# Kernel optimization log

Measured on AMD Instinct MI355X. Metric: run time of the kernel, lower is better.

Reference implementation:

```python
import jax, jax.numpy as jnp
import numpy as np
from jax import lax

B_CAPS, C_CAPS, K, STRIDE, ITERS = 32, 32, 3, 2, 3
BATCH, WIN = 8, 14
W_OUT = (WIN - K) // STRIDE + 1  # 6
CWW = C_CAPS * W_OUT * W_OUT     # 1152
LOG_2PI = float(np.log(2.0 * np.pi))


def setup_inputs() -> dict:
    key = jax.random.key(0)
    k1, k2, k3, k4, k5 = jax.random.split(key, 5)
    return {
        "poses": jax.random.normal(k1, (BATCH, B_CAPS, WIN, WIN, 16), jnp.float32),
        "activations": jax.random.uniform(k2, (BATCH, B_CAPS, WIN, WIN), jnp.float32),
        "lambda_": jnp.ones((), jnp.float32),
        "W": jax.random.normal(k3, (B_CAPS, K, K, C_CAPS, 4, 4), jnp.float32),
        "beta_v": jax.random.normal(k4, (1, CWW, 1), jnp.float32),
        "beta_a": jax.random.normal(k5, (1, CWW), jnp.float32),
    }


def reference(poses, activations, lambda_, W, beta_v, beta_a):
    b, B, win = poses.shape[0], poses.shape[1], poses.shape[2]
    C = W.shape[3]
    w = (win - K) // STRIDE + 1
    Bkk, Cww = B * K * K, C * w * w

    pose = poses.reshape(b, 16, B, win, win).transpose(0, 2, 3, 4, 1)

    # im2col patch extraction (vectorized): rows[i,k] = stride*i + k
    rows = ((jnp.arange(w) * STRIDE)[:, None] + jnp.arange(K)).reshape(-1)  # (w*K,)
    p = jnp.take(pose, rows, axis=2).reshape(b, B, w, K, win, 16)
    p = jnp.take(p, rows, axis=4).reshape(b, B, w, K, w, K, 16)
    patches = p.transpose(0, 1, 3, 5, 6, 2, 4)          # (b,B,K,K,16,wi,wj)
    # faithful reproduction of torch's view (b,B,K,K,16,ww)->(b,B,K,K,1,w,w,4,4)
    patches = patches.reshape(b, B, K, K, w, w, 4, 4)

    # votes: broadcast 4x4 matmul W @ pose-patch
    votes = jnp.einsum('sxyzij,bsxyuvjk->bsxyzuvik', W, patches)
    votes = votes.reshape(b, Bkk, Cww, 16)

    # activation patches, tiled over C (coordinate_add=False branch)
    a = jnp.take(activations, rows, axis=2).reshape(b, B, w, K, win)
    a = jnp.take(a, rows, axis=4).reshape(b, B, w, K, w, K)
    a = a.transpose(0, 1, 3, 5, 2, 4).reshape(b, Bkk, 1, w * w)
    act = jnp.broadcast_to(a, (b, Bkk, C, w * w)).reshape(b, Bkk, Cww)

    # EM routing
    R = jnp.ones((b, Bkk, Cww), votes.dtype) / Cww
    for i in range(ITERS + 1):
        Ra = (R * act)[..., None]                        # (b,Bkk,Cww,1)
        sum_R = Ra.sum(1)                                # (b,Cww,1)
        mu = ((Ra * votes).sum(1) / sum_R)[:, None]      # (b,1,Cww,16)
        sigma_sq = (Ra * (votes - mu) ** 2).sum(1) / sum_R  # (b,Cww,16)
        if i != ITERS:
            mu_d = lax.stop_gradient(mu)
            ss_d = lax.stop_gradient(sigma_sq)[:, None]  # (b,1,Cww,16)
            V_d = lax.stop_gradient(votes)
            a_d = lax.stop_gradient(act)
            log_p = -0.5 * (V_d - mu_d) ** 2 / ss_d - 0.5 * jnp.log(ss_d) - 0.5 * LOG_2PI
            ap = a_d * jnp.exp(log_p).sum(-1)            # (b,Bkk,Cww)
            R = ap / ap.sum(-1, keepdims=True)
        else:
            cost = (beta_v + jnp.log(sigma_sq)) * sum_R  # (b,Cww,16)
            a_out = jax.nn.sigmoid(lambda_ * (beta_a - cost.sum(2)))  # (b,Cww)

    return (mu.reshape(b, C, w, w, 16), a_out.reshape(b, C, w, w))
```

## Files before the change

### kernel.cpp

```cpp
#include <hip/hip_runtime.h>
#include <hip/hip_bf16.h>

#define NB   8
#define NM   288
#define NN   1152
#define NUV  36
#define ND   16

#define OFF_P    0
#define SZ_P     (NB*NUV*NM*ND)
#define OFF_WT   (OFF_P + SZ_P)
#define SZ_WT    (32*NM*ND)
#define OFF_ACT  (OFF_WT + SZ_WT)
#define SZ_ACT   (NB*NUV*NM)
#define OFF_L    (OFF_ACT + SZ_ACT)
#define SZ_L     (NB*NN*NM)
#define OFF_LSE  (OFF_L + SZ_L)
#define SZ_LSE   (NB*NM)
#define OFF_FLAG (OFF_LSE + SZ_LSE)
#define OFF_PM   (OFF_FLAG + 16)
#define SZ_PM    (NB*NUV*NM)
#define OFF_PS   (OFF_PM + SZ_PM)
#define SZ_PS    (NB*NUV*NM)

#define HALF_LOG_2PI 0.9189385332046727f
#define LOG_NN       7.049254841255839f
#define NEG_BIG      (-1.0e30f)

__device__ __forceinline__ float ldin(const void* p, int i, int f32) {
    return f32 ? ((const float*)p)[i]
               : __bfloat162float(((const __hip_bfloat16*)p)[i]);
}

__device__ __forceinline__ unsigned short bfbits(float f) {
    __hip_bfloat16 h = __float2bfloat16(f);
    return __builtin_bit_cast(unsigned short, h);
}

__device__ __forceinline__ float dot2bf(unsigned a, unsigned b, float c) {
    float d;
    asm("v_dot2_f32_bf16 %0, %1, %2, %3" : "=v"(d) : "v"(a), "v"(b), "v"(c));
    return d;
}

__global__ void detect_kernel(const unsigned short* __restrict__ poses_u16,
                              int* __restrict__ flag) {
    if (blockIdx.x == 0 && threadIdx.x == 0) {
        int wild = 0;
        for (int i = 0; i < 64; ++i) {
            int ex = (poses_u16[i] >> 7) & 0xFF;
            if (ex >= 133) ++wild;
        }
        *flag = (wild >= 4) ? 1 : 0;
    }
}

__global__ __launch_bounds__(256) void prep_kernel(
    const void* __restrict__ poses, const void* __restrict__ acts,
    const void* __restrict__ Wb, __hip_bfloat16* __restrict__ P,
    __hip_bfloat16* __restrict__ Wt, float* __restrict__ A36,
    const int* __restrict__ flagp)
{
    const int f32 = *flagp;
    const int blk = blockIdx.x;
    const int tid = threadIdx.x;
    if (blk < 256) {
        __shared__ float ps[16 * 196];
        __shared__ float asld[196];
        const int b = blk >> 5, s = blk & 31;
        for (int e = tid; e < 16 * 196; e += 256) {
            int c = e / 196, hw = e % 196;
            ps[e] = ldin(poses, ((b * 16 + c) * 32 + s) * 196 + hw, f32);
        }
        for (int e = tid; e < 196; e += 256)
            asld[e] = ldin(acts, (b * 32 + s) * 196 + e, f32);
        __syncthreads();
        for (int o2 = tid; o2 < 648; o2 += 256) {
            int row = o2 >> 1, half = o2 & 1;
            int uv = row / 9, xy = row % 9;
            int u = uv / 6, vv2 = uv % 6;
            int x = xy / 3, y = xy % 3;
            unsigned pk[4];
#pragma unroll
            for (int h = 0; h < 4; ++h) {
                unsigned lohi[2];
#pragma unroll
                for (int e = 0; e < 2; ++e) {
                    int kj = half * 8 + h * 2 + e;
                    int k = kj >> 2, j = kj & 3;
                    int idx = u * 96 + vv2 * 16 + j * 4 + k;
                    int c = idx / 36, rem = idx % 36;
                    int wi = rem / 6, wj = rem % 6;
                    lohi[e] = bfbits(ps[c * 196 + (2 * wi + x) * 14 + (2 * wj + y)]);
                }
                pk[h] = lohi[0] | (lohi[1] << 16);
            }
            *((uint4*)(P + (((size_t)((b * 36 + uv) * 288 + s * 9 + xy)) << 4) + half * 8)) =
                make_uint4(pk[0], pk[1], pk[2], pk[3]);
        }
        for (int o = tid; o < 324; o += 256) {
            int uv = o / 9, xy = o % 9;
            int u = uv / 6, vv2 = uv % 6;
            int x = xy / 3, y = xy % 3;
            A36[(b * 36 + uv) * 288 + s * 9 + xy] =
                __logf(asld[(2 * u + x) * 14 + (2 * vv2 + y)]);
        }
    } else {
        int idx = (blk - 256) * 256 + tid;
        int z = idx / 288, m = idx % 288;
        unsigned pk[8];
#pragma unroll
        for (int h = 0; h < 8; ++h) {
            unsigned lo = bfbits(ldin(Wb, m * 512 + z * 16 + 2 * h, f32));
            unsigned hi = bfbits(ldin(Wb, m * 512 + z * 16 + 2 * h + 1, f32));
            pk[h] = lo | (hi << 16);
        }
        uint4* dst = (uint4*)(Wt + idx * 16);
        dst[0] = make_uint4(pk[0], pk[1], pk[2], pk[3]);
        dst[1] = make_uint4(pk[4], pk[5], pk[6], pk[7]);
    }
}

__global__ __launch_bounds__(288, 4) void em_iter(
    const unsigned short* __restrict__ wsP, const unsigned short* __restrict__ wsWt,
    const float* __restrict__ wsA, float* __restrict__ wsL,
    const float* __restrict__ wsLSE,
    const void* __restrict__ beta_v,
    const void* __restrict__ beta_a,
    const void* __restrict__ lambda_,
    void* __restrict__ outv, const int* __restrict__ flagp, int iter)
{
    __shared__ float red[NM * 17];
    __shared__ float Mhw[9];
    __shared__ float paru[NM];
    __shared__ float parv[NM];
    __shared__ float paruW[18];
    __shared__ float mul[16], nhil[16], ltl[16], ssl[16];

    const int tid = threadIdx.x;
    const int B   = blockIdx.x;
    const int rr  = B & 255;
    const int z   = rr >> 3;
    const int g   = ((B >> 8) << 3) | (rr & 7);
    const int b   = g / NUV;
    const int uv  = g % NUV;
    const int n   = z * NUV + uv;
    const int bn  = b * NN + n;

    const uint4* Wq = (const uint4*)(wsWt + ((z * NM + tid) << 4));
    const uint4* Pq = (const uint4*)(wsP + ((g * NM + tid) << 4));
    uint4 wq0 = Wq[0], wq1 = Wq[1];
    uint4 pq0 = Pq[0], pq1 = Pq[1];
    const float lact = wsA[g * NM + tid];
    float t;
    if (iter == 0) t = lact - LOG_NN;
    else t = wsL[(size_t)bn * NM + tid] - wsLSE[b * NM + tid] + lact;
    t = fmaxf(t, NEG_BIG);

    float mhw = t;
#pragma unroll
    for (int off = 1; off < 32; off <<= 1)
        mhw = fmaxf(mhw, __shfl_xor(mhw, off, 32));
    const float w = __expf(t - mhw);
    if ((tid & 31) == 0) Mhw[tid >> 5] = mhw;

    unsigned Wa[4]  = {wq0.x, wq0.z, wq1.x, wq1.z};
    unsigned Wb_[4] = {wq0.y, wq0.w, wq1.y, wq1.w};
    unsigned Pa[4]  = {pq0.x, pq0.z, pq1.x, pq1.z};
    unsigned Pb[4]  = {pq0.y, pq0.w, pq1.y, pq1.w};
    float v[16];
#pragma unroll
    for (int i = 0; i < 4; ++i)
#pragma unroll
        for (int k = 0; k < 4; ++k)
            v[i * 4 + k] = dot2bf(Wa[i], Pa[k], dot2bf(Wb_[i], Pb[k], 0.f));

#pragma unroll
    for (int dd = 0; dd < 16; ++dd) red[tid * 17 + dd] = v[dd];
    red[tid * 17 + 16] = w;
    __syncthreads();

    {
        const int d = tid & 15, c = tid >> 4;
        const float* base = &red[(c << 4) * 17];
        float s1 = 0.f, s2 = 0.f, sw = 0.f;
#pragma unroll
        for (int q = 0; q < 16; ++q) {
            float ww = base[q * 17 + 16];
            float vv = base[q * 17 + d];
            float t1 = ww * vv;
            s1 += t1; s2 += t1 * vv; sw += ww;
        }
        paru[d * 18 + c] = s1;
        parv[d * 18 + c] = s2;
        if (d == 0) paruW[c] = sw;
    }
    __syncthreads();

    float M_f = NEG_BIG, sW_f = 0.f;
    if (tid < 16) {
        float M = Mhw[0];
#pragma unroll
        for (int h = 1; h < 9; ++h) M = fmaxf(M, Mhw[h]);
        float sW = 0.f, S1 = 0.f, S2 = 0.f;
#pragma unroll
        for (int c = 0; c < 18; ++c) {
            float sc = __expf(Mhw[c >> 1] - M);
            sW += paruW[c] * sc;
            S1 += paru[tid * 18 + c] * sc;
            S2 += parv[tid * 18 + c] * sc;
        }
        float mu = S1 / sW;
        float q2 = S2 / sW;
        float ss = fmaxf(q2 - mu * mu, 1e-30f);
        mul[tid]  = mu;
        ssl[tid]  = ss;
        nhil[tid] = -0.5f / ss;
        ltl[tid]  = -0.5f * __logf(ss) - HALF_LOG_2PI;
        M_f = M; sW_f = sW;
    }
    __syncthreads();

    if (iter < 3) {
        float lp[16];
        float M = NEG_BIG;
#pragma unroll
        for (int dd = 0; dd < 16; ++dd) {
            float df = v[dd] - mul[dd];
            lp[dd] = df * df * nhil[dd] + ltl[dd];
            M = fmaxf(M, lp[dd]);
        }
        float s = 0.f;
#pragma unroll
        for (int dd = 0; dd < 16; ++dd) s += __expf(lp[dd] - M);
        wsL[(size_t)bn * NM + tid] = lact + M + __logf(s);
    } else {
        const int f32 = *flagp;
        if (tid < 16) {
            if (f32) ((float*)outv)[(bn << 4) + tid] = mul[tid];
            else ((__hip_bfloat16*)outv)[(bn << 4) + tid] = __float2bfloat16(mul[tid]);
        }
        if (tid == 0) {
            float sumR = __expf(M_f) * sW_f;
            float bv = ldin(beta_v, n, f32);
            float c = 0.f;
#pragma unroll
            for (int dd = 0; dd < 16; ++dd) c += bv + __logf(ssl[dd]);
            c *= sumR;
            float lam = ldin(lambda_, 0, f32);
            float ba  = ldin(beta_a, n, f32);
            float ao  = 1.f / (1.f + __expf(-(lam * (ba - c))));
            int oi = NB * NN * ND + bn;
            if (f32) ((float*)outv)[oi] = ao;
            else ((__hip_bfloat16*)outv)[oi] = __float2bfloat16(ao);
        }
    }
}

__global__ __launch_bounds__(288) void lse1_kernel(const float* __restrict__ L,
                                                   float* __restrict__ PM,
                                                   float* __restrict__ PS)
{
    const int tid = threadIdx.x;
    const int blk = blockIdx.x;
    const int b = blk / NUV;
    const int c = blk % NUV;
    const float* base = L + ((size_t)b * NN + c * 32) * NM + tid;
    float mx = NEG_BIG;
#pragma unroll
    for (int r = 0; r < 32; ++r) mx = fmaxf(mx, base[r * NM]);
    float s = 0.f;
#pragma unroll
    for (int r = 0; r < 32; ++r) s += __expf(base[r * NM] - mx);
    PM[blk * NM + tid] = mx;
    PS[blk * NM + tid] = s;
}

__global__ void lse2_kernel(const float* __restrict__ PM,
                            const float* __restrict__ PS,
                            float* __restrict__ LSE)
{
    int t = blockIdx.x * 256 + threadIdx.x;
    if (t >= NB * NM) return;
    int b = t / NM, m = t % NM;
    const float* pm = PM + (size_t)b * NUV * NM + m;
    const float* ps = PS + (size_t)b * NUV * NM + m;
    float mx = NEG_BIG;
#pragma unroll
    for (int cc = 0; cc < NUV; ++cc) mx = fmaxf(mx, pm[cc * NM]);
    float s = 0.f;
#pragma unroll
    for (int cc = 0; cc < NUV; ++cc) s += ps[cc * NM] * __expf(pm[cc * NM] - mx);
    LSE[t] = mx + __logf(s);
}

extern "C" void kernel_launch(void* const* d_in, const int* in_sizes, int n_in,
                              void* d_out, int out_size, void* d_ws, size_t ws_size,
                              hipStream_t stream)
{
    const void* poses = d_in[0];
    const void* acts  = d_in[1];
    const void* lam   = d_in[2];
    const void* Wb    = d_in[3];
    const void* bv    = d_in[4];
    const void* ba    = d_in[5];

    float* ws  = (float*)d_ws;
    __hip_bfloat16* P  = (__hip_bfloat16*)(ws + OFF_P);
    __hip_bfloat16* Wt = (__hip_bfloat16*)(ws + OFF_WT);
    float* A36 = ws + OFF_ACT;
    float* L   = ws + OFF_L;
    float* LSE = ws + OFF_LSE;
    int*  flag = (int*)(ws + OFF_FLAG);
    float* PM  = ws + OFF_PM;
    float* PS  = ws + OFF_PS;

    detect_kernel<<<1, 64, 0, stream>>>((const unsigned short*)poses, flag);

    prep_kernel<<<292, 256, 0, stream>>>(poses, acts, Wb, P, Wt, A36, flag);

    for (int it = 0; it < 4; ++it) {
        em_iter<<<NB * NN, 288, 0, stream>>>((const unsigned short*)P,
                                             (const unsigned short*)Wt,
                                             A36, L, LSE, bv, ba, lam,
                                             d_out, flag, it);
        if (it < 3) {
            lse1_kernel<<<NB * NUV, 288, 0, stream>>>(L, PM, PS);
            lse2_kernel<<<9, 256, 0, stream>>>(PM, PS, LSE);
        }
    }
}
```

Measured before the change: 231.7 us.

## Process each output capsule with one wavefront using register and shuffle reductions

Each output capsule is now handled by a single 64-lane wavefront, with four capsules per 256-thread block. Each lane owns five of the 288 input rows, and the mean and variance sums are reduced with cross-lane shuffles instead of shared-memory arrays and block barriers. This removes the __syncthreads calls and the LDS traffic. In exchange, register pressure rises sharply (80 vote values plus 32 partial accumulators per lane), which risks spills or lower occupancy, and half the lanes sit idle on the fifth row chunk.

```diff
diff --git a/kernel.cpp b/kernel.cpp
--- a/kernel.cpp
+++ b/kernel.cpp
@@ -121,7 +121,7 @@
     }
 }
 
-__global__ __launch_bounds__(288, 4) void em_iter(
+__global__ __launch_bounds__(256) void em_iter(
     const unsigned short* __restrict__ wsP, const unsigned short* __restrict__ wsWt,
     const float* __restrict__ wsA, float* __restrict__ wsL,
     const float* __restrict__ wsLSE,
@@ -130,123 +130,136 @@
     const void* __restrict__ lambda_,
     void* __restrict__ outv, const int* __restrict__ flagp, int iter)
 {
-    __shared__ float red[NM * 17];
-    __shared__ float Mhw[9];
-    __shared__ float paru[NM];
-    __shared__ float parv[NM];
-    __shared__ float paruW[18];
-    __shared__ float mul[16], nhil[16], ltl[16], ssl[16];
-
-    const int tid = threadIdx.x;
-    const int B   = blockIdx.x;
-    const int rr  = B & 255;
-    const int z   = rr >> 3;
-    const int g   = ((B >> 8) << 3) | (rr & 7);
-    const int b   = g / NUV;
-    const int uv  = g % NUV;
-    const int n   = z * NUV + uv;
-    const int bn  = b * NN + n;
-
-    const uint4* Wq = (const uint4*)(wsWt + ((z * NM + tid) << 4));
-    const uint4* Pq = (const uint4*)(wsP + ((g * NM + tid) << 4));
-    uint4 wq0 = Wq[0], wq1 = Wq[1];
-    uint4 pq0 = Pq[0], pq1 = Pq[1];
-    const float lact = wsA[g * NM + tid];
-    float t;
-    if (iter == 0) t = lact - LOG_NN;
-    else t = wsL[(size_t)bn * NM + tid] - wsLSE[b * NM + tid] + lact;
-    t = fmaxf(t, NEG_BIG);
-
-    float mhw = t;
-#pragma unroll
-    for (int off = 1; off < 32; off <<= 1)
-        mhw = fmaxf(mhw, __shfl_xor(mhw, off, 32));
-    const float w = __expf(t - mhw);
-    if ((tid & 31) == 0) Mhw[tid >> 5] = mhw;
-
-    unsigned Wa[4]  = {wq0.x, wq0.z, wq1.x, wq1.z};
-    unsigned Wb_[4] = {wq0.y, wq0.w, wq1.y, wq1.w};
-    unsigned Pa[4]  = {pq0.x, pq0.z, pq1.x, pq1.z};
-    unsigned Pb[4]  = {pq0.y, pq0.w, pq1.y, pq1.w};
-    float v[16];
-#pragma unroll
-    for (int i = 0; i < 4; ++i)
-#pragma unroll
-        for (int k = 0; k < 4; ++k)
-            v[i * 4 + k] = dot2bf(Wa[i], Pa[k], dot2bf(Wb_[i], Pb[k], 0.f));
-
-#pragma unroll
-    for (int dd = 0; dd < 16; ++dd) red[tid * 17 + dd] = v[dd];
-    red[tid * 17 + 16] = w;
-    __syncthreads();
-
-    {
-        const int d = tid & 15, c = tid >> 4;
-        const float* base = &red[(c << 4) * 17];
-        float s1 = 0.f, s2 = 0.f, sw = 0.f;
-#pragma unroll
-        for (int q = 0; q < 16; ++q) {
-            float ww = base[q * 17 + 16];
-            float vv = base[q * 17 + d];
-            float t1 = ww * vv;
-            s1 += t1; s2 += t1 * vv; sw += ww;
-        }
-        paru[d * 18 + c] = s1;
-        parv[d * 18 + c] = s2;
-        if (d == 0) paruW[c] = sw;
-    }
-    __syncthreads();
-
-    float M_f = NEG_BIG, sW_f = 0.f;
-    if (tid < 16) {
-        float M = Mhw[0];
-#pragma unroll
-        for (int h = 1; h < 9; ++h) M = fmaxf(M, Mhw[h]);
-        float sW = 0.f, S1 = 0.f, S2 = 0.f;
-#pragma unroll
-        for (int c = 0; c < 18; ++c) {
-            float sc = __expf(Mhw[c >> 1] - M);
-            sW += paruW[c] * sc;
-            S1 += paru[tid * 18 + c] * sc;
-            S2 += parv[tid * 18 + c] * sc;
-        }
-        float mu = S1 / sW;
-        float q2 = S2 / sW;
-        float ss = fmaxf(q2 - mu * mu, 1e-30f);
-        mul[tid]  = mu;
-        ssl[tid]  = ss;
-        nhil[tid] = -0.5f / ss;
-        ltl[tid]  = -0.5f * __logf(ss) - HALF_LOG_2PI;
-        M_f = M; sW_f = sW;
-    }
-    __syncthreads();
+    const int tid  = threadIdx.x;
+    const int lane = tid & 63;
+    const int bn   = blockIdx.x * 4 + (tid >> 6);
+    const int b    = bn / NN;
+    const int n    = bn % NN;
+    const int z    = n / NUV;
+    const int uv   = n % NUV;
+    const int g    = b * NUV + uv;
+
+    uint4 WQ0[5], WQ1[5], PQ0[5], PQ1[5];
+#pragma unroll
+    for (int q = 0; q < 5; ++q) {
+        const int m = lane + (q << 6);
+        const uint4* Wq = (const uint4*)(wsWt + ((z * NM + m) << 4));
+        const uint4* Pq = (const uint4*)(wsP + ((g * NM + m) << 4));
+        WQ0[q] = Wq[0]; WQ1[q] = Wq[1];
+        PQ0[q] = Pq[0]; PQ1[q] = Pq[1];
+    }
+
+    const float* Arow = wsA + g * NM;
+    const float* Lrow = wsL + (size_t)bn * NM;
+    const float* Srow = wsLSE + b * NM;
+    float t[5], lact[5];
+#pragma unroll
+    for (int q = 0; q < 5; ++q) {
+        const int m = lane + (q << 6);
+        const bool on = (q < 4) || (lane < 32);
+        const float la = on ? Arow[m] : 0.f;
+        lact[q] = la;
+        float tv;
+        if (iter == 0) tv = la - LOG_NN;
+        else tv = (on ? (Lrow[m] - Srow[m]) : 0.f) + la;
+        t[q] = on ? fmaxf(tv, NEG_BIG) : NEG_BIG;
+    }
+    float M = t[0];
+#pragma unroll
+    for (int q = 1; q < 5; ++q) M = fmaxf(M, t[q]);
+#pragma unroll
+    for (int off = 1; off < 64; off <<= 1) M = fmaxf(M, __shfl_xor(M, off));
+    float w[5];
+#pragma unroll
+    for (int q = 0; q < 5; ++q) w[q] = __expf(t[q] - M);
+
+    float v[5][16];
+    float S1[16], S2[16];
+#pragma unroll
+    for (int d = 0; d < 16; ++d) { S1[d] = 0.f; S2[d] = 0.f; }
+    float sW = 0.f;
+#pragma unroll
+    for (int q = 0; q < 5; ++q) {
+        const unsigned Wa[4]  = {WQ0[q].x, WQ0[q].z, WQ1[q].x, WQ1[q].z};
+        const unsigned Wb_[4] = {WQ0[q].y, WQ0[q].w, WQ1[q].y, WQ1[q].w};
+        const unsigned Pa[4]  = {PQ0[q].x, PQ0[q].z, PQ1[q].x, PQ1[q].z};
+        const unsigned Pb[4]  = {PQ0[q].y, PQ0[q].w, PQ1[q].y, PQ1[q].w};
+        const float wq = w[q];
+        sW += wq;
+#pragma unroll
+        for (int i = 0; i < 4; ++i)
+#pragma unroll
+            for (int k = 0; k < 4; ++k) {
+                const int d = i * 4 + k;
+                float vv = dot2bf(Wa[i], Pa[k], dot2bf(Wb_[i], Pb[k], 0.f));
+                v[q][d] = vv;
+                float p = wq * vv;
+                S1[d] += p;
+                S2[d] = fmaf(p, vv, S2[d]);
+            }
+    }
+
+#pragma unroll
+    for (int off = 1; off < 64; off <<= 1) {
+        sW += __shfl_xor(sW, off);
+#pragma unroll
+        for (int d = 0; d < 16; ++d) {
+            S1[d] += __shfl_xor(S1[d], off);
+            S2[d] += __shfl_xor(S2[d], off);
+        }
+    }
+
+    const float rs = 1.f / sW;
+    float mu[16], nhi[16], ltc[16];
+    float lss = 0.f;
+#pragma unroll
+    for (int d = 0; d < 16; ++d) {
+        float m1 = S1[d] * rs;
+        float ss = fmaxf(S2[d] * rs - m1 * m1, 1e-30f);
+        float lg = __logf(ss);
+        mu[d]  = m1;
+        nhi[d] = -0.5f / ss;
+        ltc[d] = fmaf(-0.5f, lg, -HALF_LOG_2PI);
+        lss += lg;
+    }
 
     if (iter < 3) {
-        float lp[16];
-        float M = NEG_BIG;
-#pragma unroll
-        for (int dd = 0; dd < 16; ++dd) {
-            float df = v[dd] - mul[dd];
-            lp[dd] = df * df * nhil[dd] + ltl[dd];
-            M = fmaxf(M, lp[dd]);
-        }
-        float s = 0.f;
-#pragma unroll
-        for (int dd = 0; dd < 16; ++dd) s += __expf(lp[dd] - M);
-        wsL[(size_t)bn * NM + tid] = lact + M + __logf(s);
+#pragma unroll
+        for (int q = 0; q < 5; ++q) {
+            float lp[16];
+            float Mq = NEG_BIG;
+#pragma unroll
+            for (int d = 0; d < 16; ++d) {
+                float df = v[q][d] - mu[d];
+                lp[d] = fmaf(df * df, nhi[d], ltc[d]);
+                Mq = fmaxf(Mq, lp[d]);
+            }
+            float s = 0.f;
+#pragma unroll
+            for (int d = 0; d < 16; ++d) s += __expf(lp[d] - Mq);
+            if ((q < 4) || (lane < 32))
+                wsL[(size_t)bn * NM + lane + (q << 6)] = lact[q] + Mq + __logf(s);
+        }
     } else {
         const int f32 = *flagp;
-        if (tid < 16) {
-            if (f32) ((float*)outv)[(bn << 4) + tid] = mul[tid];
-            else ((__hip_bfloat16*)outv)[(bn << 4) + tid] = __float2bfloat16(mul[tid]);
-        }
-        if (tid == 0) {
-            float sumR = __expf(M_f) * sW_f;
-            float bv = ldin(beta_v, n, f32);
-            float c = 0.f;
-#pragma unroll
-            for (int dd = 0; dd < 16; ++dd) c += bv + __logf(ssl[dd]);
-            c *= sumR;
+        if (lane == 0) {
+            if (f32) {
+                float* o = (float*)outv + ((size_t)bn << 4);
+#pragma unroll
+                for (int d = 0; d < 16; ++d) o[d] = mu[d];
+            } else {
+                unsigned pk[8];
+#pragma unroll
+                for (int h = 0; h < 8; ++h)
+                    pk[h] = (unsigned)bfbits(mu[2 * h]) |
+                            ((unsigned)bfbits(mu[2 * h + 1]) << 16);
+                uint4* o = (uint4*)((__hip_bfloat16*)outv + ((size_t)bn << 4));
+                o[0] = make_uint4(pk[0], pk[1], pk[2], pk[3]);
+                o[1] = make_uint4(pk[4], pk[5], pk[6], pk[7]);
+            }
+            float sumR = __expf(M) * sW;
+            float bv  = ldin(beta_v, n, f32);
+            float c   = (16.f * bv + lss) * sumR;
             float lam = ldin(lambda_, 0, f32);
             float ba  = ldin(beta_a, n, f32);
             float ao  = 1.f / (1.f + __expf(-(lam * (ba - c))));
@@ -320,10 +333,10 @@
     prep_kernel<<<292, 256, 0, stream>>>(poses, acts, Wb, P, Wt, A36, flag);
 
     for (int it = 0; it < 4; ++it) {
-        em_iter<<<NB * NN, 288, 0, stream>>>((const unsigned short*)P,
-                                             (const unsigned short*)Wt,
-                                             A36, L, LSE, bv, ba, lam,
-                                             d_out, flag, it);
+        em_iter<<<NB * NN / 4, 256, 0, stream>>>((const unsigned short*)P,
+                                                 (const unsigned short*)Wt,
+                                                 A36, L, LSE, bv, ba, lam,
+                                                 d_out, flag, it);
         if (it < 3) {
             lse1_kernel<<<NB * NUV, 288, 0, stream>>>(L, PM, PS);
             lse2_kernel<<<9, 256, 0, stream>>>(PM, PS, LSE);
```

Measured after the change: 241.1 us. 4.1% more time.
